# Performance work log

Hardware: AMD Instinct MI355X
Metric: run time of the kernel (lower is better)

## Reference

```python
import jax, jax.numpy as jnp
import numpy as np

N, Q, P, S, B = 262144, 256, 10, 8, 4096


def setup_inputs() -> dict:
    key = jax.random.key(0)
    k1, k2, k3, k4 = jax.random.split(key, 4)
    x = jax.random.normal(k1, (N, Q), dtype=jnp.float32)
    beta_u = jax.random.normal(k2, (Q, P, S), dtype=jnp.float32)
    beta_z = jax.random.normal(k3, (Q, P, S), dtype=jnp.float32)
    seg_ids = jnp.sort(jax.random.randint(k4, (N,), 0, B, dtype=jnp.int64))
    return {"x": x, "beta_u": beta_u, "beta_z": beta_z, "seg_ids": seg_ids,
            "num_segments": B}


def reference(x, beta_u, beta_z, seg_ids, num_segments):
    # b = sqrt(mean over feature dim of beta_z^2): [1, P, S]
    b = jnp.sqrt(jnp.mean(beta_z ** 2, axis=0, keepdims=True))
    eta = beta_z / b                                   # [Q, P, S]
    # attention logits per instance: [N, P, S]
    _w = jnp.einsum('iq,qps->ips', x, beta_u)
    # scatter_softmax over instances within each bag (dim 0)
    seg_max = jax.ops.segment_max(_w, seg_ids, num_segments=num_segments)
    ex = jnp.exp(_w - seg_max[seg_ids])
    denom = jax.ops.segment_sum(ex, seg_ids, num_segments=num_segments)
    w = ex / denom[seg_ids]                            # [N, P, S]
    t = jnp.einsum('iq,qps->ips', x, eta)              # [N, P, S]
    # weighted bag pooling (segment_add_csr equivalent): [B, P, S]
    z_bag = jax.ops.segment_sum(w * t, seg_ids, num_segments=num_segments)
    mean = jnp.mean(z_bag, axis=0)
    std = jnp.std(z_bag, axis=0, ddof=1)               # torch .std is unbiased
    std = jnp.where(jnp.isnan(std), jnp.float32(1.0), std)
    return b * (z_bag - mean) / std
```

## Files before the change

### kernel.cpp

```cpp
#include <hip/hip_runtime.h>
#include <hip/hip_bf16.h>
#include <math.h>

#define NN 262144
#define QQ 256
#define PS 80
#define BB 4096
#define NSLOT 4
#define RT 64
#define NITER 8
#define SMEM_BYTES 32768

typedef _Float16 f16x8 __attribute__((ext_vector_type(8)));
typedef float f32x4  __attribute__((ext_vector_type(4)));

__device__ inline unsigned short f16b(float f) {
  return __builtin_bit_cast(unsigned short, (_Float16)f);
}
__device__ inline float f16tof(unsigned short u) {
  return (float)__builtin_bit_cast(_Float16, u);
}

__global__ void bprep_k(const float* __restrict__ bu, const float* __restrict__ bz,
                        unsigned short* __restrict__ bFlat) {
  int gid = blockIdx.x * 256 + threadIdx.x;
  if (gid >= 5120) return;
  int kt  = gid / 640;
  int rem = gid - kt * 640;
  int kg  = rem / 160;
  int c   = rem - kg * 160;
  unsigned short* dst = bFlat + (size_t)gid * 8;
  int kbase = kt * 32 + kg * 8;
#pragma unroll
  for (int j = 0; j < 8; ++j) {
    int k = kbase + j;
    float v = (c < PS) ? bu[k * PS + c] : bz[k * PS + (c - PS)];
    dst[j] = f16b(v);
  }
}

__global__ void seg_bounds_k(const int* __restrict__ seg, int* __restrict__ segstart) {
  int b = blockIdx.x * blockDim.x + threadIdx.x;
  if (b > BB) return;
  if (b == BB) { segstart[BB] = NN; return; }
  int lo = 0, hi = NN;
  while (lo < hi) {
    int mid = (lo + hi) >> 1;
    if (seg[mid] < b) lo = mid + 1; else hi = mid;
  }
  segstart[b] = lo;
}

__global__ __launch_bounds__(256, 4) void fused_k(
    const float* __restrict__ x, const unsigned short* __restrict__ bFlat,
    const int* __restrict__ seg, const int* __restrict__ segstart,
    float* __restrict__ pm, float* __restrict__ pse, float* __restrict__ pst) {
  __shared__ __align__(16) char smem[SMEM_BYTES];
  const int tid  = threadIdx.x;
  const int lane = tid & 63;
  const int wid  = tid >> 6;
  const int rs   = blockIdx.x * RT;

  const int wr   = (wid & 1) * 32;
  const int cw   = wid >> 1;
  const int lrow = lane & 15;
  const int lk16 = lane >> 4;

  {
    const int ra = tid >> 2;
    const int kg = tid & 3;
    const float* xp = x + (size_t)(rs + ra) * QQ + kg * 8;
    float4 xs[16];
#pragma unroll
    for (int kt = 0; kt < NITER; ++kt) {
      xs[2 * kt]     = *reinterpret_cast<const float4*>(xp + kt * 32);
      xs[2 * kt + 1] = *reinterpret_cast<const float4*>(xp + kt * 32 + 4);
    }
    char* dst = smem + kg * 1024 + ((ra ^ (kg << 2)) * 16);
#pragma unroll
    for (int kt = 0; kt < NITER; ++kt) {
      float4 v0 = xs[2 * kt], v1 = xs[2 * kt + 1];
      unsigned short a0 = f16b(v0.x), a1 = f16b(v0.y), a2 = f16b(v0.z), a3 = f16b(v0.w);
      unsigned short a4 = f16b(v1.x), a5 = f16b(v1.y), a6 = f16b(v1.z), a7 = f16b(v1.w);
      uint4 w = make_uint4((unsigned)a0 | ((unsigned)a1 << 16),
                           (unsigned)a2 | ((unsigned)a3 << 16),
                           (unsigned)a4 | ((unsigned)a5 << 16),
                           (unsigned)a6 | ((unsigned)a7 << 16));
      *reinterpret_cast<uint4*>(dst + kt * 4096) = w;
    }
  }
  __syncthreads();

  const unsigned short* bA = bFlat + ((size_t)lk16 * 160 + cw * 80 + lrow) * 8;
  const int aoff0 = lk16 * 1024 + (((wr + lrow)      ^ (lk16 << 2)) * 16);
  const int aoff1 = lk16 * 1024 + (((wr + 16 + lrow) ^ (lk16 << 2)) * 16);

  f16x8 br[2][5];
#define LOADB(s_, t_) do {                                                    \
    _Pragma("unroll")                                                         \
    for (int n_ = 0; n_ < 5; ++n_)                                            \
      br[s_][n_] = *reinterpret_cast<const f16x8*>(bA + (t_) * 5120 + n_ * 128); \
  } while (0)

  f32x4 acc[2][5];
#pragma unroll
  for (int m = 0; m < 2; ++m)
#pragma unroll
    for (int n = 0; n < 5; ++n) acc[m][n] = (f32x4){0.f, 0.f, 0.f, 0.f};

  LOADB(0, 0);
  LOADB(1, 1);

#pragma unroll
  for (int t = 0; t < NITER; ++t) {
    const int s = t & 1;
    f16x8 a0 = *reinterpret_cast<const f16x8*>(smem + t * 4096 + aoff0);
    f16x8 a1 = *reinterpret_cast<const f16x8*>(smem + t * 4096 + aoff1);
    __builtin_amdgcn_s_setprio(1);
#pragma unroll
    for (int n = 0; n < 5; ++n) {
      acc[0][n] = __builtin_amdgcn_mfma_f32_16x16x32_f16(a0, br[s][n], acc[0][n], 0, 0, 0);
      acc[1][n] = __builtin_amdgcn_mfma_f32_16x16x32_f16(a1, br[s][n], acc[1][n], 0, 0, 0);
    }
    __builtin_amdgcn_s_setprio(0);
    if (t < NITER - 2) LOADB(s, t + 2);
  }
#undef LOADB

  __syncthreads();
  float* res_u          = reinterpret_cast<float*>(smem);
  unsigned short* res_v = reinterpret_cast<unsigned short*>(smem + 20480);
#pragma unroll
  for (int m = 0; m < 2; ++m)
#pragma unroll
    for (int n = 0; n < 5; ++n)
#pragma unroll
      for (int rr = 0; rr < 4; ++rr) {
        int row = wr + m * 16 + lk16 * 4 + rr;
        int col = n * 16 + lrow;
        if (cw == 0) res_u[row * 80 + col] = acc[m][n][rr];
        else         res_v[row * 80 + col] = f16b(acc[m][n][rr]);
      }
  __syncthreads();

  int b0 = seg[rs];
  int b1 = seg[rs + RT - 1];
  int nu = (b1 - b0 + 1) * PS;
  for (int u = tid; u < nu; u += 256) {
    int bag = b0 + u / PS;
    int c   = u % PS;
    int sb  = segstart[bag];
    int lo  = max(sb, rs) - rs;
    int hi  = min(segstart[bag + 1], rs + RT) - rs;
    float m_ = -3.4e38f, se = 0.f, st = 0.f;
    for (int r = lo; r < hi; ++r) {
      float v  = res_u[r * 80 + c];
      float tv = f16tof(res_v[r * 80 + c]);
      float nm = fmaxf(m_, v);
      float sc = __expf(m_ - nm);
      float ee = __expf(v - nm);
      se = se * sc + ee;
      st = st * sc + ee * tv;
      m_ = nm;
    }
    int slot = blockIdx.x - (sb >> 6);
    size_t p = ((size_t)bag * NSLOT + slot) * PS + c;
    pm[p] = m_; pse[p] = se; pst[p] = st;
  }
}

__global__ __launch_bounds__(256) void combine_k(
    const int* __restrict__ segstart,
    const float* __restrict__ pm, const float* __restrict__ pse,
    const float* __restrict__ pst, float* __restrict__ zb) {
  int i = blockIdx.x * 256 + threadIdx.x;
  if (i >= BB * PS) return;
  int bag = i / PS, c = i % PS;
  int sb = segstart[bag], eb = segstart[bag + 1];
  float z = 0.f;
  if (eb > sb) {
    int ns = ((eb - 1) >> 6) - (sb >> 6) + 1;
    ns = min(ns, NSLOT);
    float m = -3.4e38f, se = 0.f, st = 0.f;
    for (int s = 0; s < ns; ++s) {
      size_t p = ((size_t)bag * NSLOT + s) * PS + c;
      float m2 = pm[p], se2 = pse[p], st2 = pst[p];
      float nm = fmaxf(m, m2);
      float s1 = __expf(m - nm);
      float s2 = __expf(m2 - nm);
      se = se * s1 + se2 * s2;
      st = st * s1 + st2 * s2;
      m = nm;
    }
    z = st / se;
  }
  zb[i] = z;
}

__device__ inline float wave_sum(float v) {
#pragma unroll
  for (int o = 32; o > 0; o >>= 1) v += __shfl_down(v, o, 64);
  return v;
}

__global__ __launch_bounds__(256) void finalize_k(
    const float* __restrict__ bz, float* __restrict__ zb_out) {
  const int c = blockIdx.x;
  const int t = threadIdx.x;

  float bvz = bz[t * PS + c];
  float bsq = bvz * bvz;

  float s = 0.f, ss = 0.f;
  for (int b = t; b < BB; b += 256) {
    float z = zb_out[b * PS + c];
    s += z;
    ss += z * z;
  }

  __shared__ float w0[4], w1[4], w2[4];
  float a0 = wave_sum(bsq);
  float a1 = wave_sum(s);
  float a2 = wave_sum(ss);
  int wid = t >> 6, lane = t & 63;
  if (lane == 0) { w0[wid] = a0; w1[wid] = a1; w2[wid] = a2; }
  __syncthreads();

  __shared__ float sh[3];
  if (t == 0) {
    float B0 = w0[0] + w0[1] + w0[2] + w0[3];
    float S1 = w1[0] + w1[1] + w1[2] + w1[3];
    float S2 = w2[0] + w2[1] + w2[2] + w2[3];
    float bval = sqrtf(B0 / (float)QQ);
    float mean = S1 / (float)BB;
    float var = (S2 - (float)BB * mean * mean) / (float)(BB - 1);
    float sd = sqrtf(fmaxf(var, 0.f));
    if (!(sd > 0.f) || sd != sd) sd = 1.f;
    sh[0] = bval; sh[1] = mean; sh[2] = sd;
  }
  __syncthreads();
  float bval = sh[0], mean = sh[1], sd = sh[2];
  for (int b = t; b < BB; b += 256) {
    zb_out[b * PS + c] = bval * (zb_out[b * PS + c] - mean) / sd;
  }
}

extern "C" void kernel_launch(void* const* d_in, const int* in_sizes, int n_in,
                              void* d_out, int out_size, void* d_ws, size_t ws_size,
                              hipStream_t stream) {
  const float* x   = (const float*)d_in[0];
  const float* bu  = (const float*)d_in[1];
  const float* bz  = (const float*)d_in[2];
  const int*   seg = (const int*)d_in[3];
  float* out = (float*)d_out;

  char* ws = (char*)d_ws;
  int* segstart         = (int*)ws;
  unsigned short* bFlat = (unsigned short*)(ws + 16640);
  size_t pn  = (size_t)BB * NSLOT * PS;
  float* pm  = (float*)(ws + 98560);
  float* pse = pm + pn;
  float* pst = pse + pn;

  bprep_k<<<20, 256, 0, stream>>>(bu, bz, bFlat);
  seg_bounds_k<<<(BB + 1 + 255) / 256, 256, 0, stream>>>(seg, segstart);
  fused_k<<<NN / RT, 256, 0, stream>>>(x, bFlat, seg, segstart, pm, pse, pst);
  combine_k<<<(BB * PS + 255) / 256, 256, 0, stream>>>(segstart, pm, pse, pst, out);
  finalize_k<<<PS, 256, 0, stream>>>(bz, out);
}
```

Measured before the change: 101.8 us.

## Split A staging into two halves overlapping MFMA, fuse combine with finalize

In the fused GEMM kernel, all x loads are issued up front, but only the first half of K is converted and written to shared memory before the first lightweight barrier. MFMAs on that half then run before the second half is written, so LDS writes overlap compute instead of sitting behind one full sync. Separately, the combine and finalize kernels are merged into one kernel with 80 blocks that keeps z in shared memory, removing a launch and a global round-trip. The risk is that the merged kernel runs only 80 blocks serially over 4096 bags, which gives low parallelism for the combine step.

```diff
diff --git a/kernel.cpp b/kernel.cpp
--- a/kernel.cpp
+++ b/kernel.cpp
@@ -20,6 +20,12 @@
 __device__ inline float f16tof(unsigned short u) {
   return (float)__builtin_bit_cast(_Float16, u);
 }
+
+#define LBAR() do {                                                           \
+    asm volatile("s_waitcnt lgkmcnt(0)" ::: "memory");                        \
+    __builtin_amdgcn_s_barrier();                                             \
+    __builtin_amdgcn_sched_barrier(0);                                        \
+  } while (0)
 
 __global__ void bprep_k(const float* __restrict__ bu, const float* __restrict__ bz,
                         unsigned short* __restrict__ bFlat) {
@@ -66,30 +72,10 @@
   const int lrow = lane & 15;
   const int lk16 = lane >> 4;
 
-  {
-    const int ra = tid >> 2;
-    const int kg = tid & 3;
-    const float* xp = x + (size_t)(rs + ra) * QQ + kg * 8;
-    float4 xs[16];
-#pragma unroll
-    for (int kt = 0; kt < NITER; ++kt) {
-      xs[2 * kt]     = *reinterpret_cast<const float4*>(xp + kt * 32);
-      xs[2 * kt + 1] = *reinterpret_cast<const float4*>(xp + kt * 32 + 4);
-    }
-    char* dst = smem + kg * 1024 + ((ra ^ (kg << 2)) * 16);
-#pragma unroll
-    for (int kt = 0; kt < NITER; ++kt) {
-      float4 v0 = xs[2 * kt], v1 = xs[2 * kt + 1];
-      unsigned short a0 = f16b(v0.x), a1 = f16b(v0.y), a2 = f16b(v0.z), a3 = f16b(v0.w);
-      unsigned short a4 = f16b(v1.x), a5 = f16b(v1.y), a6 = f16b(v1.z), a7 = f16b(v1.w);
-      uint4 w = make_uint4((unsigned)a0 | ((unsigned)a1 << 16),
-                           (unsigned)a2 | ((unsigned)a3 << 16),
-                           (unsigned)a4 | ((unsigned)a5 << 16),
-                           (unsigned)a6 | ((unsigned)a7 << 16));
-      *reinterpret_cast<uint4*>(dst + kt * 4096) = w;
-    }
-  }
-  __syncthreads();
+  const int ra = tid >> 2;
+  const int kg = tid & 3;
+  const float* xp = x + (size_t)(rs + ra) * QQ + kg * 8;
+  char* adst = smem + kg * 1024 + ((ra ^ (kg << 2)) * 16);
 
   const unsigned short* bA = bFlat + ((size_t)lk16 * 160 + cw * 80 + lrow) * 8;
   const int aoff0 = lk16 * 1024 + (((wr + lrow)      ^ (lk16 << 2)) * 16);
@@ -102,30 +88,60 @@
       br[s_][n_] = *reinterpret_cast<const f16x8*>(bA + (t_) * 5120 + n_ * 128); \
   } while (0)
 
-  f32x4 acc[2][5];
-#pragma unroll
-  for (int m = 0; m < 2; ++m)
-#pragma unroll
-    for (int n = 0; n < 5; ++n) acc[m][n] = (f32x4){0.f, 0.f, 0.f, 0.f};
-
+#define WRITEA(kt_) do {                                                      \
+    float4 v0 = xs[2 * (kt_)], v1 = xs[2 * (kt_) + 1];                        \
+    unsigned short a0 = f16b(v0.x), a1 = f16b(v0.y), a2 = f16b(v0.z), a3 = f16b(v0.w); \
+    unsigned short a4 = f16b(v1.x), a5 = f16b(v1.y), a6 = f16b(v1.z), a7 = f16b(v1.w); \
+    uint4 w = make_uint4((unsigned)a0 | ((unsigned)a1 << 16),                 \
+                         (unsigned)a2 | ((unsigned)a3 << 16),                 \
+                         (unsigned)a4 | ((unsigned)a5 << 16),                 \
+                         (unsigned)a6 | ((unsigned)a7 << 16));                \
+    *reinterpret_cast<uint4*>(adst + (kt_) * 4096) = w;                       \
+  } while (0)
+
+#define KITER(t_) do {                                                        \
+    const int s_ = (t_) & 1;                                                  \
+    f16x8 a0 = *reinterpret_cast<const f16x8*>(smem + (t_) * 4096 + aoff0);   \
+    f16x8 a1 = *reinterpret_cast<const f16x8*>(smem + (t_) * 4096 + aoff1);   \
+    __builtin_amdgcn_s_setprio(1);                                            \
+    _Pragma("unroll")                                                         \
+    for (int n_ = 0; n_ < 5; ++n_) {                                          \
+      acc[0][n_] = __builtin_amdgcn_mfma_f32_16x16x32_f16(a0, br[s_][n_], acc[0][n_], 0, 0, 0); \
+      acc[1][n_] = __builtin_amdgcn_mfma_f32_16x16x32_f16(a1, br[s_][n_], acc[1][n_], 0, 0, 0); \
+    }                                                                         \
+    __builtin_amdgcn_s_setprio(0);                                            \
+    if ((t_) < NITER - 2) LOADB(s_, (t_) + 2);                                \
+  } while (0)
+
+  float4 xs[16];
+#pragma unroll
+  for (int kt = 0; kt < NITER; ++kt) {
+    xs[2 * kt]     = *reinterpret_cast<const float4*>(xp + kt * 32);
+    xs[2 * kt + 1] = *reinterpret_cast<const float4*>(xp + kt * 32 + 4);
+  }
   LOADB(0, 0);
   LOADB(1, 1);
 
-#pragma unroll
-  for (int t = 0; t < NITER; ++t) {
-    const int s = t & 1;
-    f16x8 a0 = *reinterpret_cast<const f16x8*>(smem + t * 4096 + aoff0);
-    f16x8 a1 = *reinterpret_cast<const f16x8*>(smem + t * 4096 + aoff1);
-    __builtin_amdgcn_s_setprio(1);
-#pragma unroll
-    for (int n = 0; n < 5; ++n) {
-      acc[0][n] = __builtin_amdgcn_mfma_f32_16x16x32_f16(a0, br[s][n], acc[0][n], 0, 0, 0);
-      acc[1][n] = __builtin_amdgcn_mfma_f32_16x16x32_f16(a1, br[s][n], acc[1][n], 0, 0, 0);
-    }
-    __builtin_amdgcn_s_setprio(0);
-    if (t < NITER - 2) LOADB(s, t + 2);
-  }
+  f32x4 acc[2][5];
+#pragma unroll
+  for (int m = 0; m < 2; ++m)
+#pragma unroll
+    for (int n = 0; n < 5; ++n) acc[m][n] = (f32x4){0.f, 0.f, 0.f, 0.f};
+
+#pragma unroll
+  for (int kt = 0; kt < 4; ++kt) WRITEA(kt);
+  LBAR();
+
+  KITER(0); KITER(1); KITER(2); KITER(3);
+
+#pragma unroll
+  for (int kt = 4; kt < 8; ++kt) WRITEA(kt);
+  LBAR();
+
+  KITER(4); KITER(5); KITER(6); KITER(7);
 #undef LOADB
+#undef WRITEA
+#undef KITER
 
   __syncthreads();
   float* res_u          = reinterpret_cast<float*>(smem);
@@ -169,51 +185,45 @@
   }
 }
 
-__global__ __launch_bounds__(256) void combine_k(
+__device__ inline float wave_sum(float v) {
+#pragma unroll
+  for (int o = 32; o > 0; o >>= 1) v += __shfl_down(v, o, 64);
+  return v;
+}
+
+__global__ __launch_bounds__(256) void combfin_k(
     const int* __restrict__ segstart,
     const float* __restrict__ pm, const float* __restrict__ pse,
-    const float* __restrict__ pst, float* __restrict__ zb) {
-  int i = blockIdx.x * 256 + threadIdx.x;
-  if (i >= BB * PS) return;
-  int bag = i / PS, c = i % PS;
-  int sb = segstart[bag], eb = segstart[bag + 1];
-  float z = 0.f;
-  if (eb > sb) {
-    int ns = ((eb - 1) >> 6) - (sb >> 6) + 1;
-    ns = min(ns, NSLOT);
-    float m = -3.4e38f, se = 0.f, st = 0.f;
-    for (int s = 0; s < ns; ++s) {
-      size_t p = ((size_t)bag * NSLOT + s) * PS + c;
-      float m2 = pm[p], se2 = pse[p], st2 = pst[p];
-      float nm = fmaxf(m, m2);
-      float s1 = __expf(m - nm);
-      float s2 = __expf(m2 - nm);
-      se = se * s1 + se2 * s2;
-      st = st * s1 + st2 * s2;
-      m = nm;
-    }
-    z = st / se;
-  }
-  zb[i] = z;
-}
-
-__device__ inline float wave_sum(float v) {
-#pragma unroll
-  for (int o = 32; o > 0; o >>= 1) v += __shfl_down(v, o, 64);
-  return v;
-}
-
-__global__ __launch_bounds__(256) void finalize_k(
-    const float* __restrict__ bz, float* __restrict__ zb_out) {
+    const float* __restrict__ pst, const float* __restrict__ bz,
+    float* __restrict__ out) {
   const int c = blockIdx.x;
   const int t = threadIdx.x;
+  __shared__ float zsh[BB];
 
   float bvz = bz[t * PS + c];
   float bsq = bvz * bvz;
 
   float s = 0.f, ss = 0.f;
   for (int b = t; b < BB; b += 256) {
-    float z = zb_out[b * PS + c];
+    int sb = segstart[b], eb = segstart[b + 1];
+    float z = 0.f;
+    if (eb > sb) {
+      int ns = ((eb - 1) >> 6) - (sb >> 6) + 1;
+      ns = min(ns, NSLOT);
+      float m = -3.4e38f, se = 0.f, st = 0.f;
+      for (int sl = 0; sl < ns; ++sl) {
+        size_t p = ((size_t)b * NSLOT + sl) * PS + c;
+        float m2 = pm[p], se2 = pse[p], st2 = pst[p];
+        float nm = fmaxf(m, m2);
+        float s1 = __expf(m - nm);
+        float s2 = __expf(m2 - nm);
+        se = se * s1 + se2 * s2;
+        st = st * s1 + st2 * s2;
+        m = nm;
+      }
+      z = st / se;
+    }
+    zsh[b] = z;
     s += z;
     ss += z * z;
   }
@@ -241,7 +251,7 @@
   __syncthreads();
   float bval = sh[0], mean = sh[1], sd = sh[2];
   for (int b = t; b < BB; b += 256) {
-    zb_out[b * PS + c] = bval * (zb_out[b * PS + c] - mean) / sd;
+    out[b * PS + c] = bval * (zsh[b] - mean) / sd;
   }
 }
 
@@ -265,6 +275,5 @@
   bprep_k<<<20, 256, 0, stream>>>(bu, bz, bFlat);
   seg_bounds_k<<<(BB + 1 + 255) / 256, 256, 0, stream>>>(seg, segstart);
   fused_k<<<NN / RT, 256, 0, stream>>>(x, bFlat, seg, segstart, pm, pse, pst);
-  combine_k<<<(BB * PS + 255) / 256, 256, 0, stream>>>(segstart, pm, pse, pst, out);
-  finalize_k<<<PS, 256, 0, stream>>>(bz, out);
-}
+  combfin_k<<<PS, 256, 0, stream>>>(segstart, pm, pse, pst, bz, out);
+}
```

New measurement: 118.7 us. 1.17x slower.

## Fuse prep kernels and fuse combine with finalize normalization

Applied to the files above, without the earlier changes.

Merges the B-matrix conversion and segment-bound search into one launch, and folds the per-bag partial-softmax combine into the per-column normalization kernel. Combined values are held in shared memory, so the intermediate z_bag round trip through global memory and two launches are removed. In exchange the combine now runs in only 80 blocks with strided per-column reads of the partial buffers, which reduces parallelism and coalescing.

```diff
diff --git a/kernel.cpp b/kernel.cpp
--- a/kernel.cpp
+++ b/kernel.cpp
@@ -21,34 +21,33 @@
   return (float)__builtin_bit_cast(_Float16, u);
 }
 
-__global__ void bprep_k(const float* __restrict__ bu, const float* __restrict__ bz,
-                        unsigned short* __restrict__ bFlat) {
-  int gid = blockIdx.x * 256 + threadIdx.x;
-  if (gid >= 5120) return;
-  int kt  = gid / 640;
-  int rem = gid - kt * 640;
-  int kg  = rem / 160;
-  int c   = rem - kg * 160;
-  unsigned short* dst = bFlat + (size_t)gid * 8;
-  int kbase = kt * 32 + kg * 8;
-#pragma unroll
-  for (int j = 0; j < 8; ++j) {
-    int k = kbase + j;
-    float v = (c < PS) ? bu[k * PS + c] : bz[k * PS + (c - PS)];
-    dst[j] = f16b(v);
-  }
-}
-
-__global__ void seg_bounds_k(const int* __restrict__ seg, int* __restrict__ segstart) {
-  int b = blockIdx.x * blockDim.x + threadIdx.x;
-  if (b > BB) return;
-  if (b == BB) { segstart[BB] = NN; return; }
-  int lo = 0, hi = NN;
-  while (lo < hi) {
-    int mid = (lo + hi) >> 1;
-    if (seg[mid] < b) lo = mid + 1; else hi = mid;
-  }
-  segstart[b] = lo;
+__global__ void prep_k(const float* __restrict__ bu, const float* __restrict__ bz,
+                       unsigned short* __restrict__ bFlat,
+                       const int* __restrict__ seg, int* __restrict__ segstart) {
+  int g = blockIdx.x * 256 + threadIdx.x;
+  if (g < 5120) {
+    int kt  = g / 640;
+    int rem = g - kt * 640;
+    int kg  = rem / 160;
+    int c   = rem - kg * 160;
+    unsigned short* dst = bFlat + (size_t)g * 8;
+    int kbase = kt * 32 + kg * 8;
+#pragma unroll
+    for (int j = 0; j < 8; ++j) {
+      int k = kbase + j;
+      float v = (c < PS) ? bu[k * PS + c] : bz[k * PS + (c - PS)];
+      dst[j] = f16b(v);
+    }
+  } else if (g <= 5120 + BB) {
+    int b = g - 5120;
+    if (b == BB) { segstart[BB] = NN; return; }
+    int lo = 0, hi = NN;
+    while (lo < hi) {
+      int mid = (lo + hi) >> 1;
+      if (seg[mid] < b) lo = mid + 1; else hi = mid;
+    }
+    segstart[b] = lo;
+  }
 }
 
 __global__ __launch_bounds__(256, 4) void fused_k(
@@ -169,51 +168,45 @@
   }
 }
 
-__global__ __launch_bounds__(256) void combine_k(
+__device__ inline float wave_sum(float v) {
+#pragma unroll
+  for (int o = 32; o > 0; o >>= 1) v += __shfl_down(v, o, 64);
+  return v;
+}
+
+__global__ __launch_bounds__(256) void combfin_k(
     const int* __restrict__ segstart,
     const float* __restrict__ pm, const float* __restrict__ pse,
-    const float* __restrict__ pst, float* __restrict__ zb) {
-  int i = blockIdx.x * 256 + threadIdx.x;
-  if (i >= BB * PS) return;
-  int bag = i / PS, c = i % PS;
-  int sb = segstart[bag], eb = segstart[bag + 1];
-  float z = 0.f;
-  if (eb > sb) {
-    int ns = ((eb - 1) >> 6) - (sb >> 6) + 1;
-    ns = min(ns, NSLOT);
-    float m = -3.4e38f, se = 0.f, st = 0.f;
-    for (int s = 0; s < ns; ++s) {
-      size_t p = ((size_t)bag * NSLOT + s) * PS + c;
-      float m2 = pm[p], se2 = pse[p], st2 = pst[p];
-      float nm = fmaxf(m, m2);
-      float s1 = __expf(m - nm);
-      float s2 = __expf(m2 - nm);
-      se = se * s1 + se2 * s2;
-      st = st * s1 + st2 * s2;
-      m = nm;
-    }
-    z = st / se;
-  }
-  zb[i] = z;
-}
-
-__device__ inline float wave_sum(float v) {
-#pragma unroll
-  for (int o = 32; o > 0; o >>= 1) v += __shfl_down(v, o, 64);
-  return v;
-}
-
-__global__ __launch_bounds__(256) void finalize_k(
-    const float* __restrict__ bz, float* __restrict__ zb_out) {
+    const float* __restrict__ pst, const float* __restrict__ bz,
+    float* __restrict__ out) {
   const int c = blockIdx.x;
   const int t = threadIdx.x;
+  __shared__ float zsh[BB];
 
   float bvz = bz[t * PS + c];
   float bsq = bvz * bvz;
 
   float s = 0.f, ss = 0.f;
   for (int b = t; b < BB; b += 256) {
-    float z = zb_out[b * PS + c];
+    int sb = segstart[b], eb = segstart[b + 1];
+    float z = 0.f;
+    if (eb > sb) {
+      int ns = ((eb - 1) >> 6) - (sb >> 6) + 1;
+      ns = min(ns, NSLOT);
+      float m = -3.4e38f, se = 0.f, st = 0.f;
+      for (int sl = 0; sl < ns; ++sl) {
+        size_t p = ((size_t)b * NSLOT + sl) * PS + c;
+        float m2 = pm[p], se2 = pse[p], st2 = pst[p];
+        float nm = fmaxf(m, m2);
+        float s1 = __expf(m - nm);
+        float s2 = __expf(m2 - nm);
+        se = se * s1 + se2 * s2;
+        st = st * s1 + st2 * s2;
+        m = nm;
+      }
+      z = st / se;
+    }
+    zsh[b] = z;
     s += z;
     ss += z * z;
   }
@@ -241,7 +234,7 @@
   __syncthreads();
   float bval = sh[0], mean = sh[1], sd = sh[2];
   for (int b = t; b < BB; b += 256) {
-    zb_out[b * PS + c] = bval * (zb_out[b * PS + c] - mean) / sd;
+    out[b * PS + c] = bval * (zsh[b] - mean) / sd;
   }
 }
 
@@ -262,9 +255,7 @@
   float* pse = pm + pn;
   float* pst = pse + pn;
 
-  bprep_k<<<20, 256, 0, stream>>>(bu, bz, bFlat);
-  seg_bounds_k<<<(BB + 1 + 255) / 256, 256, 0, stream>>>(seg, segstart);
+  prep_k<<<(5120 + BB + 1 + 255) / 256, 256, 0, stream>>>(bu, bz, bFlat, seg, segstart);
   fused_k<<<NN / RT, 256, 0, stream>>>(x, bFlat, seg, segstart, pm, pse, pst);
-  combine_k<<<(BB * PS + 255) / 256, 256, 0, stream>>>(segstart, pm, pse, pst, out);
-  finalize_k<<<PS, 256, 0, stream>>>(bz, out);
-}
+  combfin_k<<<PS, 256, 0, stream>>>(segstart, pm, pse, pst, bz, out);
+}
```

Result: slower. 113.9 us (+11.9%).
